# Kernel optimization log

Measured on AMD Instinct MI355X. Metric: run time of the kernel, lower is better.

## Reference

```python
import jax, jax.numpy as jnp
import numpy as np

# Problem-size constants (match input_specs / init_kwargs)
B, D, H, W = 2, 128, 128, 128   # batch and spatial grid
N = 200_000                      # number of active (non-empty) voxels
CI, CO, K = 64, 64, 3            # channels and cubic kernel size
DIL = 1                          # dilation


def setup_inputs() -> dict:
    key = jax.random.key(0)
    k1, k2, k3 = jax.random.split(key, 3)
    # Unique active voxel coordinates (submanifold conv assumes unique sites).
    rng = np.random.default_rng(0)
    lin = rng.choice(B * D * H * W, size=N, replace=False)
    b, rem = np.divmod(lin, D * H * W)
    z, rem = np.divmod(rem, H * W)
    y, x = np.divmod(rem, W)
    coords = jnp.asarray(np.stack([b, z, y, x], axis=1).astype(np.int32))  # [N,4]
    feats = jax.random.normal(k1, (N, CI), dtype=jnp.float32)
    # kaiming-uniform-ish init, layout [Co, Kd, Kh, Kw, Ci] as in the module
    fan_in = CI * K * K * K
    bound = 1.0 / np.sqrt(fan_in)
    weight = jax.random.uniform(k2, (CO, K, K, K, CI), dtype=jnp.float32,
                                minval=-bound, maxval=bound)
    bias = jax.random.uniform(k3, (CO,), dtype=jnp.float32,
                              minval=-bound, maxval=bound)
    return {"feats": feats, "weight": weight, "bias": bias, "coords": coords}


def _build_grid(coords):
    """Dense voxel hash: linear cell id -> row index in feats (-1 if empty)."""
    n = coords.shape[0]
    lin = ((coords[:, 0] * D + coords[:, 1]) * H + coords[:, 2]) * W + coords[:, 3]
    grid = jnp.full((B * D * H * W,), -1, dtype=jnp.int32)
    return grid.at[lin].set(jnp.arange(n, dtype=jnp.int32))


def reference(feats, weight, bias, coords):
    # Submanifold sparse 3D conv: out[p] = bias + sum_k W[k] @ feats[p + dil*(k - center)]
    # (only where the neighbor voxel is active; output sites == input sites).
    n = feats.shape[0]
    grid = _build_grid(coords)
    c = K // 2
    bz, z0, y0, x0 = coords[:, 0], coords[:, 1], coords[:, 2], coords[:, 3]
    out = jnp.broadcast_to(bias.astype(feats.dtype), (n, CO))
    for kd in range(K):
        for kh in range(K):
            for kw in range(K):
                dz, dy, dx = DIL * (kd - c), DIL * (kh - c), DIL * (kw - c)
                nz, ny, nx = z0 + dz, y0 + dy, x0 + dx
                inb = (nz >= 0) & (nz < D) & (ny >= 0) & (ny < H) & (nx >= 0) & (nx < W)
                nlin = ((bz * D + jnp.clip(nz, 0, D - 1)) * H
                        + jnp.clip(ny, 0, H - 1)) * W + jnp.clip(nx, 0, W - 1)
                nidx = jnp.where(inb, grid[nlin], -1)          # rulebook for this offset
                valid = (nidx >= 0)[:, None]
                g = jnp.where(valid, feats[jnp.clip(nidx, 0)], 0.0)  # gather [N,Ci]
                out = out + jnp.einsum('nc,oc->no', g, weight[:, kd, kh, kw, :])
    return out
```

## Files before the change

kernel.cpp:

```cpp
#include <hip/hip_runtime.h>
#include <hip/hip_bf16.h>

#define BDIM 2
#define DDIM 128
#define HDIM 128
#define WDIM 128
#define CI 64
#define CO 64
#define NTAPS 27
#define GRID_CELLS (BDIM * DDIM * HDIM * WDIM)

typedef __attribute__((ext_vector_type(8))) short short8;
typedef __attribute__((ext_vector_type(4))) float floatx4;

#define GRID_BYTES 16777216
#define WT_OFF GRID_BYTES

__device__ __forceinline__ unsigned short f2bf(float f) {
    unsigned int u = __float_as_uint(f);
    return (unsigned short)((u + 0x7FFFu + ((u >> 16) & 1u)) >> 16);
}

__global__ __launch_bounds__(256) void scatter_kernel(
    const int* __restrict__ coords, int* __restrict__ grid, int n) {
    int i = blockIdx.x * blockDim.x + threadIdx.x;
    if (i >= n) return;
    int4 c = ((const int4*)coords)[i];
    grid[((c.x * DDIM + c.y) * HDIM + c.z) * WDIM + c.w] = i;
}

__global__ __launch_bounds__(256) void wfrag_kernel(
    const float* __restrict__ weight, short8* __restrict__ wt8) {
    int idx = blockIdx.x * blockDim.x + threadIdx.x;
    if (idx >= NTAPS * 2 * 4 * 64) return;
    int l = idx & 63, ot = (idx >> 6) & 3, s = (idx >> 8) & 1, t = idx >> 9;
    int o = ot * 16 + (l & 15);
    int k0 = s * 32 + ((l >> 4) << 3);
    const float* src = weight + ((size_t)o * NTAPS + t) * CI + k0;
    short8 v;
#pragma unroll
    for (int j = 0; j < 8; ++j) v[j] = (short)f2bf(src[j]);
    wt8[idx] = v;
}

__global__ __launch_bounds__(256) void fused_conv_kernel(
    const float* __restrict__ feats,
    const short8* __restrict__ wt8,
    const float* __restrict__ bias,
    const int* __restrict__ coords,
    const int* __restrict__ grid,
    float* __restrict__ out,
    int n) {
    int wave = blockIdx.x * 4 + (threadIdx.x >> 6);
    int l = threadIdx.x & 63;
    int quad = l >> 4, m = l & 15;
    int base = wave * 16;
    if (base >= n) return;

    int cpt = base + m;
    if (cpt >= n) cpt = n - 1;
    int4 c = ((const int4*)coords)[cpt];

    int p0, p1, p2, p3, p4, p5, p6;
#pragma unroll
    for (int i = 0; i < 7; ++i) {
        int t = 4 * i + quad;
        int v = -1;
        if (t < NTAPS) {
            int dz = t / 9 - 1, rem = t % 9;
            int dy = rem / 3 - 1, dx = rem % 3 - 1;
            int nz = c.y + dz, ny = c.z + dy, nx = c.w + dx;
            if (nz >= 0 && nz < DDIM && ny >= 0 && ny < HDIM &&
                nx >= 0 && nx < WDIM)
                v = grid[((c.x * DDIM + nz) * HDIM + ny) * WDIM + nx];
        }
        if (i == 0) p0 = v; else if (i == 1) p1 = v; else if (i == 2) p2 = v;
        else if (i == 3) p3 = v; else if (i == 4) p4 = v; else if (i == 5) p5 = v;
        else p6 = v;
    }

    floatx4 acc0 = {0.f, 0.f, 0.f, 0.f}, acc1 = acc0, acc2 = acc0, acc3 = acc0;

#pragma unroll
    for (int t = 0; t < NTAPS; ++t) {
        int src;
        switch (t >> 2) {
            case 0: src = p0; break; case 1: src = p1; break;
            case 2: src = p2; break; case 3: src = p3; break;
            case 4: src = p4; break; case 5: src = p5; break;
            default: src = p6; break;
        }
        int v = __shfl(src, ((t & 3) << 4) | m);
        if (__ballot(v >= 0) == 0) continue;

        float4 x0 = {0.f, 0.f, 0.f, 0.f}, x1 = x0, x2 = x0, x3 = x0;
        if (v >= 0) {
            const float4* ar = (const float4*)(feats + (size_t)v * CI + quad * 8);
            x0 = ar[0]; x1 = ar[1];
            x2 = ar[8]; x3 = ar[9];
        }
        union { short8 s; __hip_bfloat162 h[4]; } af0, af1;
        af0.h[0] = __float22bfloat162_rn({x0.x, x0.y});
        af0.h[1] = __float22bfloat162_rn({x0.z, x0.w});
        af0.h[2] = __float22bfloat162_rn({x1.x, x1.y});
        af0.h[3] = __float22bfloat162_rn({x1.z, x1.w});
        af1.h[0] = __float22bfloat162_rn({x2.x, x2.y});
        af1.h[1] = __float22bfloat162_rn({x2.z, x2.w});
        af1.h[2] = __float22bfloat162_rn({x3.x, x3.y});
        af1.h[3] = __float22bfloat162_rn({x3.z, x3.w});

        const short8* wb = wt8 + (size_t)t * 8 * 64 + l;
        acc0 = __builtin_amdgcn_mfma_f32_16x16x32_bf16(af0.s, wb[0 * 64], acc0, 0, 0, 0);
        acc1 = __builtin_amdgcn_mfma_f32_16x16x32_bf16(af0.s, wb[1 * 64], acc1, 0, 0, 0);
        acc2 = __builtin_amdgcn_mfma_f32_16x16x32_bf16(af0.s, wb[2 * 64], acc2, 0, 0, 0);
        acc3 = __builtin_amdgcn_mfma_f32_16x16x32_bf16(af0.s, wb[3 * 64], acc3, 0, 0, 0);
        acc0 = __builtin_amdgcn_mfma_f32_16x16x32_bf16(af1.s, wb[4 * 64], acc0, 0, 0, 0);
        acc1 = __builtin_amdgcn_mfma_f32_16x16x32_bf16(af1.s, wb[5 * 64], acc1, 0, 0, 0);
        acc2 = __builtin_amdgcn_mfma_f32_16x16x32_bf16(af1.s, wb[6 * 64], acc2, 0, 0, 0);
        acc3 = __builtin_amdgcn_mfma_f32_16x16x32_bf16(af1.s, wb[7 * 64], acc3, 0, 0, 0);
    }

    float b0 = bias[m], b1 = bias[m + 16], b2 = bias[m + 32], b3 = bias[m + 48];
#pragma unroll
    for (int r = 0; r < 4; ++r) {
        int pt = base + quad * 4 + r;
        if (pt < n) {
            float* orow = out + (size_t)pt * CO;
            orow[m]      = acc0[r] + b0;
            orow[m + 16] = acc1[r] + b1;
            orow[m + 32] = acc2[r] + b2;
            orow[m + 48] = acc3[r] + b3;
        }
    }
}

extern "C" void kernel_launch(void* const* d_in, const int* in_sizes, int n_in,
                              void* d_out, int out_size, void* d_ws, size_t ws_size,
                              hipStream_t stream) {
    const float* feats  = (const float*)d_in[0];
    const float* weight = (const float*)d_in[1];
    const float* bias   = (const float*)d_in[2];
    const int*   coords = (const int*)d_in[3];
    float* out = (float*)d_out;
    int n = in_sizes[3] / 4;

    int*    grid = (int*)d_ws;
    short8* wt8  = (short8*)((char*)d_ws + WT_OFF);

    hipMemsetAsync(grid, 0xFF, (size_t)GRID_CELLS * sizeof(int), stream);
    scatter_kernel<<<(n + 255) / 256, 256, 0, stream>>>(coords, grid, n);
    wfrag_kernel<<<(NTAPS * 2 * 4 * 64 + 255) / 256, 256, 0, stream>>>(weight, wt8);
    int waves = (n + 15) / 16;
    fused_conv_kernel<<<(waves + 3) / 4, 256, 0, stream>>>(
        feats, wt8, bias, coords, grid, out, n);
}
```

Baseline: 207.9 us.

## Process voxels in spatial order via grid compaction and stage weights in LDS

Adds count, scan and emit passes that compact the dense voxel grid into a spatially sorted list of point indices. The conv kernel then processes points in that order so neighbouring tiles share gathered feature rows in cache, and scatters results back to the original rows. It also triple-buffers each tap's weight fragments through shared memory with a block barrier per tap, and prefetches the next tap's feature gather into registers. The cost is two extra full-grid passes over 16 MB plus a single-block scan, and 27 block-wide syncs per tile.

```diff
diff --git a/kernel.cpp b/kernel.cpp
--- a/kernel.cpp
+++ b/kernel.cpp
@@ -9,12 +9,14 @@
 #define CO 64
 #define NTAPS 27
 #define GRID_CELLS (BDIM * DDIM * HDIM * WDIM)
+#define NCBLK (GRID_CELLS / 256)
 
 typedef __attribute__((ext_vector_type(8))) short short8;
 typedef __attribute__((ext_vector_type(4))) float floatx4;
 
-#define GRID_BYTES 16777216
-#define WT_OFF GRID_BYTES
+#define WT_OFF   ((size_t)16 << 20)
+#define BCNT_OFF (WT_OFF + ((size_t)256 << 10))
+#define ORD_OFF  (BCNT_OFF + ((size_t)64 << 10))
 
 __device__ __forceinline__ unsigned short f2bf(float f) {
     unsigned int u = __float_as_uint(f);
@@ -43,25 +45,67 @@
     wt8[idx] = v;
 }
 
-__global__ __launch_bounds__(256) void fused_conv_kernel(
-    const float* __restrict__ feats,
-    const short8* __restrict__ wt8,
-    const float* __restrict__ bias,
-    const int* __restrict__ coords,
-    const int* __restrict__ grid,
-    float* __restrict__ out,
-    int n) {
-    int wave = blockIdx.x * 4 + (threadIdx.x >> 6);
-    int l = threadIdx.x & 63;
-    int quad = l >> 4, m = l & 15;
-    int base = wave * 16;
-    if (base >= n) return;
-
-    int cpt = base + m;
-    if (cpt >= n) cpt = n - 1;
-    int4 c = ((const int4*)coords)[cpt];
-
-    int p0, p1, p2, p3, p4, p5, p6;
+__global__ __launch_bounds__(256) void count_kernel(
+    const int* __restrict__ grid, int* __restrict__ bcnt) {
+    int i = blockIdx.x * 256 + threadIdx.x;
+    unsigned long long b = __ballot(grid[i] >= 0);
+    __shared__ int wc[4];
+    if ((threadIdx.x & 63) == 0) wc[threadIdx.x >> 6] = __popcll(b);
+    __syncthreads();
+    if (threadIdx.x == 0) bcnt[blockIdx.x] = wc[0] + wc[1] + wc[2] + wc[3];
+}
+
+__global__ __launch_bounds__(1024) void scan_kernel(int* __restrict__ bcnt) {
+    __shared__ int part[1024];
+    int tid = threadIdx.x;
+    int v[16], s = 0;
+#pragma unroll
+    for (int k = 0; k < 16; ++k) { v[k] = bcnt[tid * 16 + k]; s += v[k]; }
+    part[tid] = s;
+    __syncthreads();
+    for (int off = 1; off < 1024; off <<= 1) {
+        int t = (tid >= off) ? part[tid - off] : 0;
+        __syncthreads();
+        part[tid] += t;
+        __syncthreads();
+    }
+    int ex = tid ? part[tid - 1] : 0;
+#pragma unroll
+    for (int k = 0; k < 16; ++k) { int nv = ex; ex += v[k]; bcnt[tid * 16 + k] = nv; }
+}
+
+__global__ __launch_bounds__(256) void emit_kernel(
+    const int* __restrict__ grid, const int* __restrict__ boff,
+    int* __restrict__ order) {
+    int i = blockIdx.x * 256 + threadIdx.x;
+    int v = grid[i];
+    int lane = threadIdx.x & 63, w = threadIdx.x >> 6;
+    unsigned long long b = __ballot(v >= 0);
+    __shared__ int wc[4];
+    if (lane == 0) wc[w] = __popcll(b);
+    __syncthreads();
+    int woff = 0;
+    for (int k = 0; k < w; ++k) woff += wc[k];
+    if (v >= 0) {
+        int rank = __popcll(b & ((1ull << lane) - 1ull));
+        order[boff[blockIdx.x] + woff + rank] = v;
+    }
+}
+
+__global__ __launch_bounds__(256) void conv_kernel(
+    const float* __restrict__ feats, const short8* __restrict__ wt8,
+    const float* __restrict__ bias, const int* __restrict__ coords,
+    const int* __restrict__ grid, const int* __restrict__ order,
+    float* __restrict__ out, int n) {
+    __shared__ short8 bs[3][512];
+    int tid = threadIdx.x;
+    int w = tid >> 6, l = tid & 63, quad = l >> 4, m = l & 15;
+    int jrow = blockIdx.x * 64 + w * 16 + m;
+    int j = jrow < n ? jrow : n - 1;
+    int p = order[j];
+    int4 c = ((const int4*)coords)[p];
+
+    int pr[7];
 #pragma unroll
     for (int i = 0; i < 7; ++i) {
         int t = 4 * i + quad;
@@ -74,64 +118,84 @@
                 nx >= 0 && nx < WDIM)
                 v = grid[((c.x * DDIM + nz) * HDIM + ny) * WDIM + nx];
         }
-        if (i == 0) p0 = v; else if (i == 1) p1 = v; else if (i == 2) p2 = v;
-        else if (i == 3) p3 = v; else if (i == 4) p4 = v; else if (i == 5) p5 = v;
-        else p6 = v;
+        pr[i] = v;
     }
 
     floatx4 acc0 = {0.f, 0.f, 0.f, 0.f}, acc1 = acc0, acc2 = acc0, acc3 = acc0;
-
+    float4 xA[4], xB[4];
+    int vA = -1, vB = -1;
+
+#define STAGE(t)                                                     \
+    {                                                                \
+        const short8* src = wt8 + (size_t)(t) * 512 + tid * 2;       \
+        short8 s0 = src[0], s1 = src[1];                             \
+        bs[(t) % 3][tid * 2] = s0;                                   \
+        bs[(t) % 3][tid * 2 + 1] = s1;                               \
+    }
+
+#define GATHER(t, g, vv)                                             \
+    {                                                                \
+        int vsrc = pr[(t) >> 2];                                     \
+        vv = __shfl(vsrc, (((t) & 3) << 4) | m);                     \
+        g[0] = g[1] = g[2] = g[3] = float4{0.f, 0.f, 0.f, 0.f};      \
+        if (vv >= 0) {                                               \
+            const float4* ar =                                       \
+                (const float4*)(feats + (size_t)vv * CI + quad * 8); \
+            g[0] = ar[0]; g[1] = ar[1]; g[2] = ar[8]; g[3] = ar[9];  \
+        }                                                            \
+    }
+
+#define COMPUTE(t, g, vv)                                                          \
+    if (__ballot(vv >= 0) != 0ull) {                                               \
+        union { short8 s; __hip_bfloat162 h[4]; } f0, f1;                          \
+        f0.h[0] = __float22bfloat162_rn({g[0].x, g[0].y});                         \
+        f0.h[1] = __float22bfloat162_rn({g[0].z, g[0].w});                         \
+        f0.h[2] = __float22bfloat162_rn({g[1].x, g[1].y});                         \
+        f0.h[3] = __float22bfloat162_rn({g[1].z, g[1].w});                         \
+        f1.h[0] = __float22bfloat162_rn({g[2].x, g[2].y});                         \
+        f1.h[1] = __float22bfloat162_rn({g[2].z, g[2].w});                         \
+        f1.h[2] = __float22bfloat162_rn({g[3].x, g[3].y});                         \
+        f1.h[3] = __float22bfloat162_rn({g[3].z, g[3].w});                         \
+        const short8* wb = &bs[(t) % 3][l];                                        \
+        acc0 = __builtin_amdgcn_mfma_f32_16x16x32_bf16(f0.s, wb[0 * 64], acc0, 0, 0, 0); \
+        acc1 = __builtin_amdgcn_mfma_f32_16x16x32_bf16(f0.s, wb[1 * 64], acc1, 0, 0, 0); \
+        acc2 = __builtin_amdgcn_mfma_f32_16x16x32_bf16(f0.s, wb[2 * 64], acc2, 0, 0, 0); \
+        acc3 = __builtin_amdgcn_mfma_f32_16x16x32_bf16(f0.s, wb[3 * 64], acc3, 0, 0, 0); \
+        acc0 = __builtin_amdgcn_mfma_f32_16x16x32_bf16(f1.s, wb[4 * 64], acc0, 0, 0, 0); \
+        acc1 = __builtin_amdgcn_mfma_f32_16x16x32_bf16(f1.s, wb[5 * 64], acc1, 0, 0, 0); \
+        acc2 = __builtin_amdgcn_mfma_f32_16x16x32_bf16(f1.s, wb[6 * 64], acc2, 0, 0, 0); \
+        acc3 = __builtin_amdgcn_mfma_f32_16x16x32_bf16(f1.s, wb[7 * 64], acc3, 0, 0, 0); \
+    }
+
+    STAGE(0);
+    GATHER(0, xA, vA);
 #pragma unroll
     for (int t = 0; t < NTAPS; ++t) {
-        int src;
-        switch (t >> 2) {
-            case 0: src = p0; break; case 1: src = p1; break;
-            case 2: src = p2; break; case 3: src = p3; break;
-            case 4: src = p4; break; case 5: src = p5; break;
-            default: src = p6; break;
+        if (t + 1 < NTAPS) {
+            STAGE(t + 1);
+            if (t & 1) { GATHER(t + 1, xA, vA); } else { GATHER(t + 1, xB, vB); }
         }
-        int v = __shfl(src, ((t & 3) << 4) | m);
-        if (__ballot(v >= 0) == 0) continue;
-
-        float4 x0 = {0.f, 0.f, 0.f, 0.f}, x1 = x0, x2 = x0, x3 = x0;
-        if (v >= 0) {
-            const float4* ar = (const float4*)(feats + (size_t)v * CI + quad * 8);
-            x0 = ar[0]; x1 = ar[1];
-            x2 = ar[8]; x3 = ar[9];
-        }
-        union { short8 s; __hip_bfloat162 h[4]; } af0, af1;
-        af0.h[0] = __float22bfloat162_rn({x0.x, x0.y});
-        af0.h[1] = __float22bfloat162_rn({x0.z, x0.w});
-        af0.h[2] = __float22bfloat162_rn({x1.x, x1.y});
-        af0.h[3] = __float22bfloat162_rn({x1.z, x1.w});
-        af1.h[0] = __float22bfloat162_rn({x2.x, x2.y});
-        af1.h[1] = __float22bfloat162_rn({x2.z, x2.w});
-        af1.h[2] = __float22bfloat162_rn({x3.x, x3.y});
-        af1.h[3] = __float22bfloat162_rn({x3.z, x3.w});
-
-        const short8* wb = wt8 + (size_t)t * 8 * 64 + l;
-        acc0 = __builtin_amdgcn_mfma_f32_16x16x32_bf16(af0.s, wb[0 * 64], acc0, 0, 0, 0);
-        acc1 = __builtin_amdgcn_mfma_f32_16x16x32_bf16(af0.s, wb[1 * 64], acc1, 0, 0, 0);
-        acc2 = __builtin_amdgcn_mfma_f32_16x16x32_bf16(af0.s, wb[2 * 64], acc2, 0, 0, 0);
-        acc3 = __builtin_amdgcn_mfma_f32_16x16x32_bf16(af0.s, wb[3 * 64], acc3, 0, 0, 0);
-        acc0 = __builtin_amdgcn_mfma_f32_16x16x32_bf16(af1.s, wb[4 * 64], acc0, 0, 0, 0);
-        acc1 = __builtin_amdgcn_mfma_f32_16x16x32_bf16(af1.s, wb[5 * 64], acc1, 0, 0, 0);
-        acc2 = __builtin_amdgcn_mfma_f32_16x16x32_bf16(af1.s, wb[6 * 64], acc2, 0, 0, 0);
-        acc3 = __builtin_amdgcn_mfma_f32_16x16x32_bf16(af1.s, wb[7 * 64], acc3, 0, 0, 0);
+        __syncthreads();
+        if (t & 1) { COMPUTE(t, xB, vB); } else { COMPUTE(t, xA, vA); }
     }
 
     float b0 = bias[m], b1 = bias[m + 16], b2 = bias[m + 32], b3 = bias[m + 48];
 #pragma unroll
     for (int r = 0; r < 4; ++r) {
-        int pt = base + quad * 4 + r;
-        if (pt < n) {
-            float* orow = out + (size_t)pt * CO;
+        int row = quad * 4 + r;
+        int jr = blockIdx.x * 64 + w * 16 + row;
+        int prow = __shfl(p, row);
+        if (jr < n) {
+            float* orow = out + (size_t)prow * CO;
             orow[m]      = acc0[r] + b0;
             orow[m + 16] = acc1[r] + b1;
             orow[m + 32] = acc2[r] + b2;
             orow[m + 48] = acc3[r] + b3;
         }
     }
+#undef STAGE
+#undef GATHER
+#undef COMPUTE
 }
 
 extern "C" void kernel_launch(void* const* d_in, const int* in_sizes, int n_in,
@@ -144,13 +208,17 @@
     float* out = (float*)d_out;
     int n = in_sizes[3] / 4;
 
-    int*    grid = (int*)d_ws;
-    short8* wt8  = (short8*)((char*)d_ws + WT_OFF);
-
-    hipMemsetAsync(grid, 0xFF, (size_t)GRID_CELLS * sizeof(int), stream);
+    int*    grid  = (int*)d_ws;
+    short8* wt8   = (short8*)((char*)d_ws + WT_OFF);
+    int*    bcnt  = (int*)((char*)d_ws + BCNT_OFF);
+    int*    order = (int*)((char*)d_ws + ORD_OFF);
+
+    (void)hipMemsetAsync(grid, 0xFF, (size_t)GRID_CELLS * sizeof(int), stream);
     scatter_kernel<<<(n + 255) / 256, 256, 0, stream>>>(coords, grid, n);
     wfrag_kernel<<<(NTAPS * 2 * 4 * 64 + 255) / 256, 256, 0, stream>>>(weight, wt8);
-    int waves = (n + 15) / 16;
-    fused_conv_kernel<<<(waves + 3) / 4, 256, 0, stream>>>(
-        feats, wt8, bias, coords, grid, out, n);
-}
+    count_kernel<<<NCBLK, 256, 0, stream>>>(grid, bcnt);
+    scan_kernel<<<1, 1024, 0, stream>>>(bcnt);
+    emit_kernel<<<NCBLK, 256, 0, stream>>>(grid, bcnt, order);
+    conv_kernel<<<(n + 63) / 64, 256, 0, stream>>>(
+        feats, wt8, bias, coords, grid, order, out, n);
+}
```

New measurement: 195.8 us. 1.06x faster.
